# Kernel tuning notes

Measured on AMD Instinct MI355X. Metric: run time of the kernel, lower is better.

Reference implementation:

```python
import jax, jax.numpy as jnp
import numpy as np

# Module configuration (from init_kwargs)
N, C_IN, C_OUT, L, V, P = 4, 64, 64, 1024, 25, 3
KERNEL_SIZE, STRIDE = 9, 1
EPS = 1e-5


def _toeplitz(length):
    # Faithful to: sum_i pad(eye(L - stride*i), (i*stride, 0, 0, i*stride))
    # -> ones at [r, r + i*stride] for i in range(kernel_size // stride)
    t = jnp.zeros((length, length), dtype=jnp.float32)
    for i in range(KERNEL_SIZE // STRIDE):  # small fixed loop over taps
        t = t + jnp.eye(length, k=i * STRIDE, dtype=jnp.float32)
    return t


def setup_inputs() -> dict:
    key = jax.random.key(0)
    k0, k1, k2, k3 = jax.random.split(key, 4)
    x = jax.random.normal(k0, (N, C_IN, L, V), dtype=jnp.float32)
    A = jax.random.uniform(k1, (P, V, V), dtype=jnp.float32)
    edge_importance = jnp.ones((P, V, V), dtype=jnp.float32)
    conv_w = jax.random.normal(k2, (C_OUT * P, C_IN, 1, 1), dtype=jnp.float32) * 0.05
    conv_b = jax.random.normal(k3, (C_OUT * P,), dtype=jnp.float32) * 0.05
    gamma = jnp.ones((C_OUT,), dtype=jnp.float32)
    beta = jnp.zeros((C_OUT,), dtype=jnp.float32)
    return {"x": x, "A": A, "edge_importance": edge_importance,
            "conv_w": conv_w, "conv_b": conv_b, "gamma": gamma, "beta": beta}


def reference(x, A, edge_importance, conv_w, conv_b, gamma, beta):
    n, _, l, v = x.shape
    res = x  # residual: in_channels == out_channels and stride == 1 -> identity

    # 1x1 conv: (N, C_in, L, V) -> (N, P*C_out, L, V)
    w = conv_w[:, :, 0, 0]  # (P*C_out, C_in)
    y = jnp.einsum('nclv,kc->nklv', x, w) + conv_b[None, :, None, None]

    # split into P chunks of C_out along channels, stack, permute -> (N, L, P, C_out, V)
    y = y.reshape(n, P, C_OUT, l, v).transpose(0, 3, 1, 2, 4)

    # partition-wise graph adjacency matmul with edge-importance mask
    y = jnp.einsum('nlpcv,pvw->nlpcw', y, A * edge_importance)

    # Toeplitz temporal conv: (N, P, C, V, L) @ (L, L)
    y = y.transpose(0, 2, 3, 4, 1)
    y = jnp.matmul(y, _toeplitz(l))
    y = y.sum(axis=1)            # sum over partitions -> (N, C, V, L)
    y = y.transpose(0, 1, 3, 2)  # (N, C, L, V)

    # BatchNorm2d with batch statistics (track_running_stats=False) + ReLU
    mean = y.mean(axis=(0, 2, 3), keepdims=True)
    var = y.var(axis=(0, 2, 3), keepdims=True)  # biased, as torch uses for normalization
    y = (y - mean) * jax.lax.rsqrt(var + EPS)
    y = y * gamma[None, :, None, None] + beta[None, :, None, None]
    y = jax.nn.relu(y)

    # do = Sequential(ReLU, Dropout(0.0)) applied to (y + res)
    return jax.nn.relu(y + res)
```

## Files before the change

kernel.cpp:

```cpp
#include <hip/hip_runtime.h>


typedef unsigned short ushort_t;
typedef __attribute__((ext_vector_type(8))) short short8;
typedef __attribute__((ext_vector_type(4))) float f32x4;
typedef __attribute__((ext_vector_type(4))) unsigned short us4;

#define N_  4
#define CI_ 64
#define CO_ 64
#define L_  1024
#define V_  25
#define P_  3
#define KS_ 9
#define NLV 102400.0f
#define NREP 128
#define TSTR 406

__device__ __forceinline__ float b2f(ushort_t u) {
  union { float f; unsigned int i; } c; c.i = ((unsigned int)u) << 16; return c.f;
}
__device__ __forceinline__ ushort_t f2b(float f) {
  union { float f; unsigned int i; } c; c.f = f;
  unsigned int u = c.i;
  u += 0x7fffu + ((u >> 16) & 1u);
  return (ushort_t)(u >> 16);
}

__global__ __launch_bounds__(256) void kwin(
    const float* __restrict__ x, ushort_t* __restrict__ xs,
    const float* __restrict__ A, const float* __restrict__ E,
    const float* __restrict__ cb, const float* __restrict__ W,
    ushort_t* __restrict__ a2raw, float* __restrict__ biastab,
    ushort_t* __restrict__ wb, float* __restrict__ statsbuf)
{
  const int chunk = blockIdx.x;
  const int n = blockIdx.y;
  const int tid = threadIdx.x;

  if (chunk == 128) {
    if (n != 0) return;
    __shared__ float colA[P_ * 32];
    if (tid < P_ * 32) {
      int p = tid >> 5, w = tid & 31;
      float s = 0.f;
      if (w < V_)
        for (int v = 0; v < V_; ++v) {
          int idx = (p * V_ + v) * V_ + w;
          s += A[idx] * E[idx];
        }
      colA[tid] = s;
    }
    for (int e = tid; e < 32 * 96; e += 256) {
      int w = e / 96, k = e - w * 96;
      int p = k >> 5, v = k & 31;
      float val = 0.f;
      if (w < V_ && v < V_) {
        int idx = (p * V_ + v) * V_ + w;
        val = A[idx] * E[idx];
      }
      a2raw[e] = f2b(val);
    }
    for (int e = tid; e < 192 * 64; e += 256) wb[e] = f2b(W[e]);
    __syncthreads();
    for (int e = tid; e < 32 * 64; e += 256) {
      int w = e >> 6, c = e & 63;
      float s = 0.f;
      for (int p = 0; p < P_; ++p) s += cb[p * 64 + c] * colA[p * 32 + w];
      biastab[e] = s;
    }
    for (int e = tid; e < NREP * 128; e += 256) statsbuf[e] = 0.f;
    return;
  }

  __shared__ __align__(16) ushort_t tile[64 * TSTR];
  const int l0 = chunk * 8;
  const long xn = (long)n * CI_ * L_ * V_;
  for (int m = tid; m < 6400; m += 256) {
    int ci = m / 100;
    int j4 = (m - ci * 100) * 4;
    f32x4 d;
    if (chunk == 0 && j4 < 200) {
      d = (f32x4){0.f, 0.f, 0.f, 0.f};
    } else {
      d = *(const f32x4*)(x + xn + (long)ci * (L_ * V_) + (l0 - 8) * V_ + j4);
    }
    unsigned int p0 = (unsigned int)f2b(d[0]) | ((unsigned int)f2b(d[1]) << 16);
    unsigned int p1 = (unsigned int)f2b(d[2]) | ((unsigned int)f2b(d[3]) << 16);
    *(unsigned int*)(&tile[ci * TSTR + j4])     = p0;
    *(unsigned int*)(&tile[ci * TSTR + j4 + 2]) = p1;
  }
  __syncthreads();
  const long xsbase = ((long)n * L_ + l0) * 1600;
  for (int cp = tid; cp < 800; cp += 256) {
    const int v = cp >> 5, ci = (cp & 31) * 2;
    const ushort_t* c0 = &tile[ci * TSTR + v];
    const ushort_t* c1 = c0 + TSTR;
    float s0 = 0.f, s1 = 0.f;
#pragma unroll
    for (int li = 0; li < 9; ++li) { s0 += b2f(c0[li * 25]); s1 += b2f(c1[li * 25]); }
    *(unsigned int*)(xs + xsbase + v * 64 + ci) =
        (unsigned int)f2b(s0) | ((unsigned int)f2b(s1) << 16);
#pragma unroll
    for (int l_ = 1; l_ < 8; ++l_) {
      s0 += b2f(c0[(l_ + 8) * 25]) - b2f(c0[(l_ - 1) * 25]);
      s1 += b2f(c1[(l_ + 8) * 25]) - b2f(c1[(l_ - 1) * 25]);
      *(unsigned int*)(xs + xsbase + l_ * 1600 + v * 64 + ci) =
          (unsigned int)f2b(s0) | ((unsigned int)f2b(s1) << 16);
    }
  }
}

__global__ __launch_bounds__(256, 4) void kmain(
    const ushort_t* __restrict__ xs,
    const ushort_t* __restrict__ Wb,
    const ushort_t* __restrict__ a2,
    const float*    __restrict__ biastab,
    ushort_t*       __restrict__ zb,
    float*          __restrict__ statsbuf)
{
  const int lb = blockIdx.x;
  const int n  = blockIdx.y;
  const int tid = threadIdx.x, lane = tid & 63, wv = tid >> 6;
  const int m16 = lane & 15, quad = lane >> 4;

  __shared__ __align__(16) ushort_t T1[13312];

  const ushort_t* xsb = xs + ((long)n * L_ + 4 * lb) * 1600;

  short8 bfr[2][4][2];
#pragma unroll
  for (int pair = 0; pair < 2; ++pair)
#pragma unroll
    for (int nt = 0; nt < 4; ++nt) {
      const int v = (nt & 1) * 16 + m16;
      const int l_ = pair * 2 + (nt >> 1);
#pragma unroll
      for (int ks = 0; ks < 2; ++ks) {
        short8 t = (short8){0, 0, 0, 0, 0, 0, 0, 0};
        if (v < V_)
          t = *(const short8*)(xsb + l_ * 1600 + v * 64 + ks * 32 + quad * 8);
        bfr[pair][nt][ks] = t;
      }
    }

  short8 af[3][2];
#pragma unroll
  for (int i = 0; i < 3; ++i) {
    const ushort_t* wrow = Wb + ((wv * 3 + i) * 16 + m16) * 64 + quad * 8;
    af[i][0] = *(const short8*)(wrow);
    af[i][1] = *(const short8*)(wrow + 32);
  }

  const int cbase = wv * 16 + quad * 4;
  float s1[4] = {0.f, 0.f, 0.f, 0.f}, s2[4] = {0.f, 0.f, 0.f, 0.f};

#pragma unroll
  for (int pair = 0; pair < 2; ++pair) {
    if (pair) __syncthreads();

#pragma unroll
    for (int i = 0; i < 3; ++i) {
      f32x4 acc[4];
#pragma unroll
      for (int nt = 0; nt < 4; ++nt) acc[nt] = (f32x4){0.f, 0.f, 0.f, 0.f};
#pragma unroll
      for (int nt = 0; nt < 4; ++nt) {
        acc[nt] = __builtin_amdgcn_mfma_f32_16x16x32_bf16(af[i][0], bfr[pair][nt][0], acc[nt], 0, 0, 0);
        acc[nt] = __builtin_amdgcn_mfma_f32_16x16x32_bf16(af[i][1], bfr[pair][nt][1], acc[nt], 0, 0, 0);
      }
      const int mt = wv * 3 + i;
#pragma unroll
      for (int nt = 0; nt < 4; ++nt) {
        const int l_ = nt >> 1;
        const int col = (nt & 1) * 16 + m16;
#pragma unroll
        for (int r = 0; r < 4; ++r) {
          int k = mt * 16 + quad * 4 + r;
          T1[l_ * 6656 + (k & 63) * 104 + (k >> 6) * 32 + col] = f2b(acc[nt][r]);
        }
      }
    }
    __syncthreads();

    short8 bfr2[2][3];
#pragma unroll
    for (int nt = 0; nt < 2; ++nt)
#pragma unroll
      for (int ks = 0; ks < 3; ++ks)
        bfr2[nt][ks] = *(const short8*)(a2 + (nt * 16 + m16) * 96 + ks * 32 + quad * 8);

    f32x4 acc2[2][2];
#pragma unroll
    for (int l_ = 0; l_ < 2; ++l_)
#pragma unroll
      for (int nt = 0; nt < 2; ++nt) acc2[l_][nt] = (f32x4){0.f, 0.f, 0.f, 0.f};

#pragma unroll
    for (int l_ = 0; l_ < 2; ++l_)
#pragma unroll
      for (int ks = 0; ks < 3; ++ks) {
        short8 afT = *(const short8*)(&T1[l_ * 6656 + (wv * 16 + m16) * 104 + ks * 32 + quad * 8]);
        acc2[l_][0] = __builtin_amdgcn_mfma_f32_16x16x32_bf16(afT, bfr2[0][ks], acc2[l_][0], 0, 0, 0);
        acc2[l_][1] = __builtin_amdgcn_mfma_f32_16x16x32_bf16(afT, bfr2[1][ks], acc2[l_][1], 0, 0, 0);
      }

#pragma unroll
    for (int l_ = 0; l_ < 2; ++l_) {
      const int l = 4 * lb + pair * 2 + l_;
      const float cnt = (float)(l + 1 < KS_ ? l + 1 : KS_);
#pragma unroll
      for (int nt = 0; nt < 2; ++nt) {
        const int w = nt * 16 + m16;
        if (w < V_) {
          f32x4 bias = *(const f32x4*)(biastab + w * 64 + cbase);
          us4 pack;
#pragma unroll
          for (int r = 0; r < 4; ++r) {
            pack[r] = f2b(acc2[l_][nt][r] + cnt * bias[r]);
            float zr = b2f(pack[r]);
            s1[r] += zr; s2[r] += zr * zr;
          }
          *(us4*)(&zb[(((long)(n * L_ + l) * V_ + w) << 6) + cbase]) = pack;
        }
      }
    }
  }
#pragma unroll
  for (int off = 1; off < 16; off <<= 1) {
#pragma unroll
    for (int r = 0; r < 4; ++r) {
      s1[r] += __shfl_xor(s1[r], off, 64);
      s2[r] += __shfl_xor(s2[r], off, 64);
    }
  }
  if (m16 == 0) {
    float* sb = statsbuf + ((n * 256 + lb) & (NREP - 1)) * 128;
#pragma unroll
    for (int r = 0; r < 4; ++r) {
      atomicAdd(&sb[cbase + r], s1[r]);
      atomicAdd(&sb[64 + cbase + r], s2[r]);
    }
  }
}

__global__ __launch_bounds__(256) void kapply(
    const ushort_t* __restrict__ zb, const float* __restrict__ x,
    const float* __restrict__ statsbuf,
    const float* __restrict__ gamma, const float* __restrict__ beta,
    float* __restrict__ out)
{
  const int n = blockIdx.y, chunk = blockIdx.x;
  const int tid = threadIdx.x;
  __shared__ __align__(16) ushort_t zl[200 * 66];
  __shared__ f32x4 red[8][32];
  __shared__ float sc[64], sh[64];
  const long zbase = (long)((n * L_ + chunk * 8) * V_) * 64;
  for (int m = tid; m < 6400; m += 256) {
    const int row = m >> 5, c2 = (m & 31) * 2;
    const int cs = c2 ^ (((row >> 2) & 31) << 1);
    *(unsigned int*)(&zl[row * 66 + cs]) = ((const unsigned int*)(zb + zbase))[m];
  }
  {
    const int s4 = tid & 31, grp = tid >> 5;
    const f32x4* sb4 = (const f32x4*)statsbuf;
    f32x4 a = (f32x4){0.f, 0.f, 0.f, 0.f};
    for (int k = grp; k < NREP; k += 8) {
      f32x4 v = sb4[k * 32 + s4];
      a[0] += v[0]; a[1] += v[1]; a[2] += v[2]; a[3] += v[3];
    }
    red[grp][s4] = a;
  }
  __syncthreads();
  if (tid < 64) {
    const float inv = 1.0f / NLV;
    float s = 0.f, sq = 0.f;
#pragma unroll
    for (int g = 0; g < 8; ++g) {
      s  += red[g][tid >> 2][tid & 3];
      sq += red[g][16 + (tid >> 2)][tid & 3];
    }
    float mean = s * inv;
    float var  = sq * inv - mean * mean;
    float rstd = rsqrtf(var + 1e-5f);
    float g = gamma[tid];
    sc[tid] = rstd * g;
    sh[tid] = beta[tid] - mean * rstd * g;
  }
  __syncthreads();
  const long obase = ((long)(n * 64) * L_ + chunk * 8) * V_;
  for (int m = tid; m < 3200; m += 256) {
    int c = m / 50, q = m - c * 50, rr = q * 4;
    const int e = ((q & 31) << 1);
    long xi = obase + (long)c * (L_ * V_) + rr;
    f32x4 xv = *(const f32x4*)(x + xi);
    const float scc = sc[c], shc = sh[c];
    f32x4 o;
#pragma unroll
    for (int j = 0; j < 4; ++j) {
      float z = b2f(zl[(rr + j) * 66 + (c ^ e)]);
      float y = fmaxf(z * scc + shc, 0.f);
      o[j] = fmaxf(y + xv[j], 0.f);
    }
    *(f32x4*)(out + xi) = o;
  }
}

extern "C" void kernel_launch(void* const* d_in, const int* in_sizes, int n_in,
                              void* d_out, int out_size, void* d_ws, size_t ws_size,
                              hipStream_t stream)
{
  const float* x     = (const float*)d_in[0];
  const float* A     = (const float*)d_in[1];
  const float* E     = (const float*)d_in[2];
  const float* W     = (const float*)d_in[3];
  const float* cb    = (const float*)d_in[4];
  const float* gamma = (const float*)d_in[5];
  const float* beta  = (const float*)d_in[6];
  float* out = (float*)d_out;

  char* ws = (char*)d_ws;
  const size_t XS_OFF   = 0;
  const size_t ZB_OFF   = 13107200;
  const size_t WB_OFF   = 26214400;
  const size_t A2_OFF   = WB_OFF + 32768;
  const size_t BIAS_OFF = A2_OFF + 16384;
  const size_t STAT_OFF = BIAS_OFF + 16384;
  ushort_t* xs       = (ushort_t*)(ws + XS_OFF);
  ushort_t* zb       = (ushort_t*)(ws + ZB_OFF);
  ushort_t* wb       = (ushort_t*)(ws + WB_OFF);
  ushort_t* a2       = (ushort_t*)(ws + A2_OFF);
  float*    biastab  = (float*)(ws + BIAS_OFF);
  float*    statsbuf = (float*)(ws + STAT_OFF);

  kwin  <<<dim3(129, N_), 256, 0, stream>>>(x, xs, A, E, cb, W, a2, biastab, wb,
                                            statsbuf);
  kmain <<<dim3(256, N_), 256, 0, stream>>>(xs, wb, a2, biastab, zb, statsbuf);
  kapply<<<dim3(128, N_), 256, 0, stream>>>(zb, x, statsbuf, gamma, beta, out);
}
```

Before: 138.7 us.

## Fuse BN apply into main kernel via cooperative grid sync

The main MFMA kernel becomes a cooperative launch. Each block keeps its bf16 outputs in LDS, prefetches its residual x tile, waits on a grid-wide barrier for the batch statistics, then applies BN, ReLU and the residual directly. This removes the zb round trip through global memory and the separate apply launch. The window kernel also splits its channels across twice as many blocks, and fewer stats replicas are used. The cost is a grid barrier that needs all 1024 blocks resident at once (4 per CU), with a fallback to the old path when that is not possible.

```diff
diff --git a/kernel.cpp b/kernel.cpp
--- a/kernel.cpp
+++ b/kernel.cpp
@@ -1,4 +1,7 @@
 #include <hip/hip_runtime.h>
+#include <hip/hip_cooperative_groups.h>
+
+namespace cg = cooperative_groups;
 
 
 typedef unsigned short ushort_t;
@@ -14,7 +17,7 @@
 #define P_  3
 #define KS_ 9
 #define NLV 102400.0f
-#define NREP 128
+#define NREP 32
 #define TSTR 406
 
 __device__ __forceinline__ float b2f(ushort_t u) {
@@ -34,11 +37,11 @@
     ushort_t* __restrict__ a2raw, float* __restrict__ biastab,
     ushort_t* __restrict__ wb, float* __restrict__ statsbuf)
 {
-  const int chunk = blockIdx.x;
+  const int bx = blockIdx.x;
   const int n = blockIdx.y;
   const int tid = threadIdx.x;
 
-  if (chunk == 128) {
+  if (bx == 256) {
     if (n != 0) return;
     __shared__ float colA[P_ * 32];
     if (tid < P_ * 32) {
@@ -73,10 +76,11 @@
     return;
   }
 
-  __shared__ __align__(16) ushort_t tile[64 * TSTR];
+  const int chunk = bx >> 1, half = bx & 1;
+  __shared__ __align__(16) ushort_t tile[32 * TSTR];
   const int l0 = chunk * 8;
-  const long xn = (long)n * CI_ * L_ * V_;
-  for (int m = tid; m < 6400; m += 256) {
+  const long xn = (long)n * CI_ * L_ * V_ + (long)(half * 32) * (L_ * V_);
+  for (int m = tid; m < 3200; m += 256) {
     int ci = m / 100;
     int j4 = (m - ci * 100) * 4;
     f32x4 d;
@@ -91,9 +95,9 @@
     *(unsigned int*)(&tile[ci * TSTR + j4 + 2]) = p1;
   }
   __syncthreads();
-  const long xsbase = ((long)n * L_ + l0) * 1600;
-  for (int cp = tid; cp < 800; cp += 256) {
-    const int v = cp >> 5, ci = (cp & 31) * 2;
+  const long xsbase = ((long)n * L_ + l0) * 1600 + half * 32;
+  for (int cp = tid; cp < 400; cp += 256) {
+    const int v = cp >> 4, ci = (cp & 15) * 2;
     const ushort_t* c0 = &tile[ci * TSTR + v];
     const ushort_t* c1 = c0 + TSTR;
     float s0 = 0.f, s1 = 0.f;
@@ -111,13 +115,18 @@
   }
 }
 
+template<bool COOP>
 __global__ __launch_bounds__(256, 4) void kmain(
     const ushort_t* __restrict__ xs,
     const ushort_t* __restrict__ Wb,
     const ushort_t* __restrict__ a2,
     const float*    __restrict__ biastab,
     ushort_t*       __restrict__ zb,
-    float*          __restrict__ statsbuf)
+    float*          __restrict__ statsbuf,
+    const float*    __restrict__ gamma,
+    const float*    __restrict__ beta,
+    const float*    __restrict__ x,
+    float*          __restrict__ out)
 {
   const int lb = blockIdx.x;
   const int n  = blockIdx.y;
@@ -126,11 +135,22 @@
 
   __shared__ __align__(16) ushort_t T1[13312];
 
+  short8 af[3][2];
+#pragma unroll
+  for (int i = 0; i < 3; ++i) {
+    const ushort_t* wrow = Wb + ((wv * 3 + i) * 16 + m16) * 64 + quad * 8;
+    af[i][0] = *(const short8*)(wrow);
+    af[i][1] = *(const short8*)(wrow + 32);
+  }
+
   const ushort_t* xsb = xs + ((long)n * L_ + 4 * lb) * 1600;
-
-  short8 bfr[2][4][2];
-#pragma unroll
-  for (int pair = 0; pair < 2; ++pair)
+  const int cbase = wv * 16 + quad * 4;
+  float s1[4] = {0.f, 0.f, 0.f, 0.f}, s2[4] = {0.f, 0.f, 0.f, 0.f};
+  us4 zpack[2][2][2];
+
+#pragma unroll
+  for (int pair = 0; pair < 2; ++pair) {
+    short8 bfr[4][2];
 #pragma unroll
     for (int nt = 0; nt < 4; ++nt) {
       const int v = (nt & 1) * 16 + m16;
@@ -140,35 +160,27 @@
         short8 t = (short8){0, 0, 0, 0, 0, 0, 0, 0};
         if (v < V_)
           t = *(const short8*)(xsb + l_ * 1600 + v * 64 + ks * 32 + quad * 8);
-        bfr[pair][nt][ks] = t;
-      }
-    }
-
-  short8 af[3][2];
-#pragma unroll
-  for (int i = 0; i < 3; ++i) {
-    const ushort_t* wrow = Wb + ((wv * 3 + i) * 16 + m16) * 64 + quad * 8;
-    af[i][0] = *(const short8*)(wrow);
-    af[i][1] = *(const short8*)(wrow + 32);
-  }
-
-  const int cbase = wv * 16 + quad * 4;
-  float s1[4] = {0.f, 0.f, 0.f, 0.f}, s2[4] = {0.f, 0.f, 0.f, 0.f};
-
-#pragma unroll
-  for (int pair = 0; pair < 2; ++pair) {
+        bfr[nt][ks] = t;
+      }
+    }
+
+    f32x4 acc1[3][4];
+#pragma unroll
+    for (int i = 0; i < 3; ++i)
+#pragma unroll
+      for (int j = 0; j < 4; ++j) acc1[i][j] = (f32x4){0.f, 0.f, 0.f, 0.f};
+
+#pragma unroll
+    for (int i = 0; i < 3; ++i)
+#pragma unroll
+      for (int nt = 0; nt < 4; ++nt) {
+        acc1[i][nt] = __builtin_amdgcn_mfma_f32_16x16x32_bf16(af[i][0], bfr[nt][0], acc1[i][nt], 0, 0, 0);
+        acc1[i][nt] = __builtin_amdgcn_mfma_f32_16x16x32_bf16(af[i][1], bfr[nt][1], acc1[i][nt], 0, 0, 0);
+      }
+
     if (pair) __syncthreads();
-
 #pragma unroll
     for (int i = 0; i < 3; ++i) {
-      f32x4 acc[4];
-#pragma unroll
-      for (int nt = 0; nt < 4; ++nt) acc[nt] = (f32x4){0.f, 0.f, 0.f, 0.f};
-#pragma unroll
-      for (int nt = 0; nt < 4; ++nt) {
-        acc[nt] = __builtin_amdgcn_mfma_f32_16x16x32_bf16(af[i][0], bfr[pair][nt][0], acc[nt], 0, 0, 0);
-        acc[nt] = __builtin_amdgcn_mfma_f32_16x16x32_bf16(af[i][1], bfr[pair][nt][1], acc[nt], 0, 0, 0);
-      }
       const int mt = wv * 3 + i;
 #pragma unroll
       for (int nt = 0; nt < 4; ++nt) {
@@ -177,7 +189,7 @@
 #pragma unroll
         for (int r = 0; r < 4; ++r) {
           int k = mt * 16 + quad * 4 + r;
-          T1[l_ * 6656 + (k & 63) * 104 + (k >> 6) * 32 + col] = f2b(acc[nt][r]);
+          T1[l_ * 6656 + (k & 63) * 104 + (k >> 6) * 32 + col] = f2b(acc1[i][nt][r]);
         }
       }
     }
@@ -221,7 +233,10 @@
             float zr = b2f(pack[r]);
             s1[r] += zr; s2[r] += zr * zr;
           }
-          *(us4*)(&zb[(((long)(n * L_ + l) * V_ + w) << 6) + cbase]) = pack;
+          if constexpr (COOP)
+            zpack[pair][l_][nt] = pack;
+          else
+            *(us4*)(&zb[(((long)(n * L_ + l) * V_ + w) << 6) + cbase]) = pack;
         }
       }
     }
@@ -240,6 +255,84 @@
     for (int r = 0; r < 4; ++r) {
       atomicAdd(&sb[cbase + r], s1[r]);
       atomicAdd(&sb[64 + cbase + r], s2[r]);
+    }
+  }
+
+  if constexpr (COOP) {
+    __syncthreads();
+    ushort_t* zl = T1;
+#pragma unroll
+    for (int pair = 0; pair < 2; ++pair)
+#pragma unroll
+      for (int l_ = 0; l_ < 2; ++l_)
+#pragma unroll
+        for (int nt = 0; nt < 2; ++nt) {
+          const int w = nt * 16 + m16;
+          if (w < V_) {
+            const int rr = (pair * 2 + l_) * 25 + w;
+            const int e = ((rr >> 2) & 31) << 1;
+            const us4 pk = zpack[pair][l_][nt];
+            *(unsigned int*)(&zl[rr * 68 + (cbase ^ e)]) =
+                (unsigned int)pk[0] | ((unsigned int)pk[1] << 16);
+            *(unsigned int*)(&zl[rr * 68 + ((cbase + 2) ^ e)]) =
+                (unsigned int)pk[2] | ((unsigned int)pk[3] << 16);
+          }
+        }
+
+    const long obase = (long)(n * 64) * (L_ * V_) + lb * 100;
+    f32x4 xv[7];
+#pragma unroll
+    for (int i = 0; i < 7; ++i) {
+      const int m = tid + i * 256;
+      if (m < 1600) {
+        const int c = m / 25, q = m - c * 25;
+        xv[i] = *(const f32x4*)(x + obase + (long)c * (L_ * V_) + q * 4);
+      }
+    }
+
+    cg::this_grid().sync();
+
+    float* part = (float*)&T1[8192];
+    float* scsh = (float*)&T1[8704];
+    {
+      const int slot = tid & 127, hf = tid >> 7;
+      float a = 0.f;
+      for (int k = hf; k < NREP; k += 2)
+        a += __hip_atomic_load(&statsbuf[k * 128 + slot],
+                               __ATOMIC_RELAXED, __HIP_MEMORY_SCOPE_AGENT);
+      part[tid] = a;
+    }
+    __syncthreads();
+    if (tid < 64) {
+      const float inv = 1.0f / NLV;
+      float s    = part[tid]      + part[128 + tid];
+      float sq   = part[64 + tid] + part[192 + tid];
+      float mean = s * inv;
+      float var  = sq * inv - mean * mean;
+      float rstd = rsqrtf(var + 1e-5f);
+      float g = gamma[tid];
+      scsh[tid]      = rstd * g;
+      scsh[64 + tid] = beta[tid] - mean * rstd * g;
+    }
+    __syncthreads();
+
+#pragma unroll
+    for (int i = 0; i < 7; ++i) {
+      const int m = tid + i * 256;
+      if (m < 1600) {
+        const int c = m / 25, q = m - c * 25, rr = q * 4;
+        const int e = q << 1;
+        const long xi = obase + (long)c * (L_ * V_) + rr;
+        const float scc = scsh[c], shc = scsh[64 + c];
+        f32x4 o;
+#pragma unroll
+        for (int j = 0; j < 4; ++j) {
+          float z = b2f(zl[(rr + j) * 68 + (c ^ e)]);
+          float y = fmaxf(z * scc + shc, 0.f);
+          o[j] = fmaxf(y + xv[i][j], 0.f);
+        }
+        *(f32x4*)(out + xi) = o;
+      }
     }
   }
 }
@@ -333,8 +426,25 @@
   float*    biastab  = (float*)(ws + BIAS_OFF);
   float*    statsbuf = (float*)(ws + STAT_OFF);
 
-  kwin  <<<dim3(129, N_), 256, 0, stream>>>(x, xs, A, E, cb, W, a2, biastab, wb,
-                                            statsbuf);
-  kmain <<<dim3(256, N_), 256, 0, stream>>>(xs, wb, a2, biastab, zb, statsbuf);
-  kapply<<<dim3(128, N_), 256, 0, stream>>>(zb, x, statsbuf, gamma, beta, out);
-}
+  kwin<<<dim3(257, N_), 256, 0, stream>>>(x, xs, A, E, cb, W, a2, biastab, wb,
+                                          statsbuf);
+
+  auto kcoop = kmain<true>;
+  int maxb = 0;
+  hipError_t qe = hipOccupancyMaxActiveBlocksPerMultiprocessor(&maxb, kcoop, 256, 0);
+  bool coop = (qe == hipSuccess) && (maxb >= 4);
+
+  if (coop) {
+    void* args[] = {&xs, &wb, &a2, &biastab, &zb, &statsbuf,
+                    (void*)&gamma, (void*)&beta, (void*)&x, &out};
+    hipError_t le = hipLaunchCooperativeKernel((const void*)kcoop,
+                                               dim3(256, N_), dim3(256),
+                                               args, 0, stream);
+    if (le != hipSuccess) coop = false;
+  }
+  if (!coop) {
+    kmain<false><<<dim3(256, N_), 256, 0, stream>>>(
+        xs, wb, a2, biastab, zb, statsbuf, gamma, beta, x, out);
+    kapply<<<dim3(128, N_), 256, 0, stream>>>(zb, x, statsbuf, gamma, beta, out);
+  }
+}
```

Result: faster. 129.4 us (-6.7%).
